# Kernel optimization log

Hardware: AMD Instinct MI355X
Metric: run time of the kernel (lower is better)

The kernel has to match this reference:

```python
import jax, jax.numpy as jnp
import numpy as np

HIDDEN = 512
MEM = 512
COMM = 512
N = 8192


def setup_inputs() -> dict:
    key = jax.random.key(0)
    ks = jax.random.split(key, 8)
    in_dim = HIDDEN + MEM
    s = 1.0 / np.sqrt(in_dim)
    return {
        "u": jax.random.normal(ks[0], (N, HIDDEN), dtype=jnp.float32),
        "z": jax.random.normal(ks[1], (N, MEM), dtype=jnp.float32),
        # torch Linear weights have shape (out, in); biases init to 0 per _init_weights
        "Wk": jax.random.normal(ks[2], (COMM, in_dim), dtype=jnp.float32) * s,
        "bk": jnp.zeros((COMM,), dtype=jnp.float32),
        "Wv": jax.random.normal(ks[3], (COMM, in_dim), dtype=jnp.float32) * s,
        "bv": jnp.zeros((COMM,), dtype=jnp.float32),
        "Wq": jax.random.normal(ks[4], (COMM, in_dim), dtype=jnp.float32) * s,
        "bq": jnp.zeros((COMM,), dtype=jnp.float32),
    }


def reference(u, z, Wk, bk, Wv, bv, Wq, bq):
    n = u.shape[0]
    scale = jnp.sqrt(jnp.asarray(Wk.shape[0], dtype=u.dtype))
    s = jnp.concatenate([u, z], axis=-1)              # (N, in_dim)
    keys = s @ Wk.T + bk                              # (N, C)
    values = s @ Wv.T + bv                            # (N, C)
    queries = s @ Wq.T + bq                           # (N, C)
    scores = (queries @ keys.T) / scale               # (N, N)
    eye = jnp.eye(n, dtype=bool)
    scores = jnp.where(eye, -jnp.inf, scores)         # self-mask
    comm_attn = jax.nn.softmax(scores, axis=-1)
    comm_attn = jnp.nan_to_num(comm_attn, nan=0.0)
    m_bar = comm_attn @ values                        # (N, C)
    return (m_bar, comm_attn)
```

## Files before the change

### kernel.cpp

```cpp
#include <hip/hip_runtime.h>
#include <hip/hip_bf16.h>
#include <stdint.h>

#define N_TOK 8192
#define IN_DIM 1024
#define CDIM 512
#define NW 1536

typedef short bf16x8 __attribute__((ext_vector_type(8)));
typedef float f32x4 __attribute__((ext_vector_type(4)));

__device__ __forceinline__ unsigned short f2bf(float f) {
  union { float f; unsigned int u; } x; x.f = f;
  unsigned int u = x.u;
  u += 0x7fffu + ((u >> 16) & 1u);
  return (unsigned short)(u >> 16);
}

#define GLD16(g, l) __builtin_amdgcn_global_load_lds( \
    (const __attribute__((address_space(1))) void*)(g), \
    (__attribute__((address_space(3))) void*)(l), 16, 0, 0)

__global__ __launch_bounds__(256) void k_convert(
    const float* __restrict__ u, const float* __restrict__ z,
    const float* __restrict__ wk, const float* __restrict__ wv,
    const float* __restrict__ wq,
    ushort* __restrict__ Sb, ushort* __restrict__ Wb) {
  const int S4 = N_TOK * IN_DIM / 4;
  const int W4 = NW * IN_DIM / 4;
  const int total = S4 + W4;
  for (int e = blockIdx.x * blockDim.x + threadIdx.x; e < total;
       e += gridDim.x * blockDim.x) {
    float4 v; ushort* dst;
    if (e < S4) {
      int idx = e << 2; int row = idx >> 10; int col = idx & 1023;
      const float* src = (col < 512) ? (u + row * 512 + col)
                                     : (z + row * 512 + (col - 512));
      v = *(const float4*)src;
      dst = Sb + idx;
    } else {
      int idx = (e - S4) << 2; int row = idx >> 10; int col = idx & 1023;
      const float* base = (row < 512) ? wk : (row < 1024 ? wv : wq);
      v = *(const float4*)(base + (size_t)(row & 511) * 1024 + col);
      dst = Wb + idx;
    }
    ushort4 o;
    o.x = f2bf(v.x); o.y = f2bf(v.y); o.z = f2bf(v.z); o.w = f2bf(v.w);
    *(ushort4*)dst = o;
  }
}

__global__ __launch_bounds__(256) void k_kvq(
    const ushort* __restrict__ Sb, const ushort* __restrict__ Wb,
    const float* __restrict__ bk, const float* __restrict__ bv,
    const float* __restrict__ bq,
    ushort* __restrict__ Kb, ushort* __restrict__ Qb, ushort* __restrict__ VT) {
  __shared__ __align__(16) ushort As[128 * 64];
  __shared__ __align__(16) ushort Bs[128 * 64];
  const int tid = threadIdx.x, lane = tid & 63, w = tid >> 6;
  const int wr = w >> 1, wc = w & 1;
  const int tm = blockIdx.x, tn = blockIdx.y;

  f32x4 acc[4][4];
#pragma unroll
  for (int m = 0; m < 4; m++)
#pragma unroll
    for (int n = 0; n < 4; n++) acc[m][n] = (f32x4){0.f, 0.f, 0.f, 0.f};

  const ushort* ga0 = Sb + (size_t)tm * 128 * IN_DIM;
  const ushort* gb0 = Wb + (size_t)tn * 128 * IN_DIM;

  for (int k0 = 0; k0 < IN_DIM; k0 += 64) {
#pragma unroll
    for (int i = 0; i < 4; i++) {
      int e = i * 256 + tid;
      int row = e >> 3, c8 = (e & 7) << 3;
      GLD16(ga0 + (size_t)row * IN_DIM + k0 + c8, As + e * 8);
      GLD16(gb0 + (size_t)row * IN_DIM + k0 + c8, Bs + e * 8);
    }
    __syncthreads();
#pragma unroll
    for (int kb = 0; kb < 2; kb++) {
      bf16x8 af[4], bfr[4];
#pragma unroll
      for (int m = 0; m < 4; m++)
        af[m] = *(const bf16x8*)(As + (wr * 64 + m * 16 + (lane & 15)) * 64 +
                                 kb * 32 + ((lane >> 4) << 3));
#pragma unroll
      for (int n = 0; n < 4; n++)
        bfr[n] = *(const bf16x8*)(Bs + (wc * 64 + n * 16 + (lane & 15)) * 64 +
                                  kb * 32 + ((lane >> 4) << 3));
#pragma unroll
      for (int m = 0; m < 4; m++)
#pragma unroll
        for (int n = 0; n < 4; n++)
          acc[m][n] = __builtin_amdgcn_mfma_f32_16x16x32_bf16(af[m], bfr[n],
                                                              acc[m][n], 0, 0, 0);
    }
    __syncthreads();
  }

  const int region = tn >> 2;
  const int colr = (tn & 3) * 128 + wc * 64;
  const int rbase = tm * 128 + wr * 64;
  const float* bias = (region == 0) ? bk : (region == 1 ? bv : bq);
  if (region == 1) {
#pragma unroll
    for (int m = 0; m < 4; m++) {
      int r0 = rbase + m * 16 + ((lane >> 4) << 2);
#pragma unroll
      for (int n = 0; n < 4; n++) {
        int c = colr + n * 16 + (lane & 15);
        float b = bias[c];
        ushort4 pk;
        pk.x = f2bf(acc[m][n][0] + b);
        pk.y = f2bf(acc[m][n][1] + b);
        pk.z = f2bf(acc[m][n][2] + b);
        pk.w = f2bf(acc[m][n][3] + b);
        *(ushort4*)(VT + (size_t)c * N_TOK + r0) = pk;
      }
    }
  } else {
    ushort* O = (region == 0) ? Kb : Qb;
#pragma unroll
    for (int m = 0; m < 4; m++) {
      int r0 = rbase + m * 16 + ((lane >> 4) << 2);
#pragma unroll
      for (int n = 0; n < 4; n++) {
        int c = colr + n * 16 + (lane & 15);
        float b = bias[c];
#pragma unroll
        for (int rg = 0; rg < 4; rg++)
          O[(size_t)(r0 + rg) * CDIM + c] = f2bf(acc[m][n][rg] + b);
      }
    }
  }
}

__global__ __launch_bounds__(256) void k_scores(
    const ushort* __restrict__ Qb, const ushort* __restrict__ Kb,
    float* __restrict__ E, float* __restrict__ rowpart) {
  __shared__ __align__(16) ushort As[128 * 64];
  __shared__ __align__(16) ushort Bs[128 * 64];
  __shared__ float sums[256];
  const int tid = threadIdx.x, lane = tid & 63, w = tid >> 6;
  const int wr = w >> 1, wc = w & 1;
  const int tm = blockIdx.x, tn = blockIdx.y;

  f32x4 acc[4][4];
#pragma unroll
  for (int m = 0; m < 4; m++)
#pragma unroll
    for (int n = 0; n < 4; n++) acc[m][n] = (f32x4){0.f, 0.f, 0.f, 0.f};

  const ushort* ga0 = Qb + (size_t)tm * 128 * CDIM;
  const ushort* gb0 = Kb + (size_t)tn * 128 * CDIM;

  for (int k0 = 0; k0 < CDIM; k0 += 64) {
#pragma unroll
    for (int i = 0; i < 4; i++) {
      int e = i * 256 + tid;
      int row = e >> 3, c8 = (e & 7) << 3;
      GLD16(ga0 + (size_t)row * CDIM + k0 + c8, As + e * 8);
      GLD16(gb0 + (size_t)row * CDIM + k0 + c8, Bs + e * 8);
    }
    __syncthreads();
#pragma unroll
    for (int kb = 0; kb < 2; kb++) {
      bf16x8 af[4], bfr[4];
#pragma unroll
      for (int m = 0; m < 4; m++)
        af[m] = *(const bf16x8*)(As + (wr * 64 + m * 16 + (lane & 15)) * 64 +
                                 kb * 32 + ((lane >> 4) << 3));
#pragma unroll
      for (int n = 0; n < 4; n++)
        bfr[n] = *(const bf16x8*)(Bs + (wc * 64 + n * 16 + (lane & 15)) * 64 +
                                  kb * 32 + ((lane >> 4) << 3));
#pragma unroll
      for (int m = 0; m < 4; m++)
#pragma unroll
        for (int n = 0; n < 4; n++)
          acc[m][n] = __builtin_amdgcn_mfma_f32_16x16x32_bf16(af[m], bfr[n],
                                                              acc[m][n], 0, 0, 0);
    }
    __syncthreads();
  }

  const float scale = 0.044194173824159216f;
  float rs[4][4];
#pragma unroll
  for (int m = 0; m < 4; m++)
#pragma unroll
    for (int rg = 0; rg < 4; rg++) rs[m][rg] = 0.f;

#pragma unroll
  for (int m = 0; m < 4; m++) {
    int grow_b = tm * 128 + wr * 64 + m * 16 + ((lane >> 4) << 2);
#pragma unroll
    for (int n = 0; n < 4; n++) {
      int gcol = tn * 128 + wc * 64 + n * 16 + (lane & 15);
#pragma unroll
      for (int rg = 0; rg < 4; rg++) {
        int grow = grow_b + rg;
        float ev = (grow == gcol) ? 0.0f : __expf(acc[m][n][rg] * scale);
        E[(size_t)grow * N_TOK + gcol] = ev;
        rs[m][rg] += ev;
      }
    }
  }
#pragma unroll
  for (int m = 0; m < 4; m++)
#pragma unroll
    for (int rg = 0; rg < 4; rg++) {
      float s = rs[m][rg];
      s += __shfl_xor(s, 1);
      s += __shfl_xor(s, 2);
      s += __shfl_xor(s, 4);
      s += __shfl_xor(s, 8);
      rs[m][rg] = s;
    }
  if ((lane & 15) == 0) {
#pragma unroll
    for (int m = 0; m < 4; m++)
#pragma unroll
      for (int rg = 0; rg < 4; rg++)
        sums[wc * 128 + wr * 64 + m * 16 + ((lane >> 4) << 2) + rg] = rs[m][rg];
  }
  __syncthreads();
  if (tid < 128)
    rowpart[(size_t)(tm * 128 + tid) * 64 + tn] = sums[tid] + sums[128 + tid];
}

__global__ __launch_bounds__(256) void k_rcp(const float* __restrict__ rowpart,
                                             float* __restrict__ rcp_l) {
  int row = blockIdx.x * blockDim.x + threadIdx.x;
  if (row < N_TOK) {
    const float4* p = (const float4*)(rowpart + (size_t)row * 64);
    float s = 0.f;
#pragma unroll
    for (int i = 0; i < 16; i++) {
      float4 v = p[i];
      s += v.x + v.y + v.z + v.w;
    }
    rcp_l[row] = 1.0f / s;
  }
}

__global__ __launch_bounds__(512) void k_attn_pv(
    float* __restrict__ EA,
    const ushort* __restrict__ VT, const float* __restrict__ rcp_l,
    float* __restrict__ part) {
  __shared__ __align__(16) ushort Ps[64 * 64];
  const int tid = threadIdx.x, lane = tid & 63, w = tid >> 6;
  const int rb = blockIdx.x * 64;
  const int jc = blockIdx.y;
  const size_t jbase = (size_t)jc * 4096;

  f32x4 acc[4][4];
#pragma unroll
  for (int m = 0; m < 4; m++)
#pragma unroll
    for (int n = 0; n < 4; n++) acc[m][n] = (f32x4){0.f, 0.f, 0.f, 0.f};

  const int lrow = tid >> 3;
  const int tr = tid & 7;
  const float rl = rcp_l[rb + lrow];
  float* erow = EA + (size_t)(rb + lrow) * N_TOK + jbase + tr * 8;

  float4 e0 = *(const float4*)(erow);
  float4 e1 = *(const float4*)(erow + 4);

  for (int jt = 0; jt < 64; ++jt) {
    float4 p0, p1;
    p0.x = e0.x * rl; p0.y = e0.y * rl; p0.z = e0.z * rl; p0.w = e0.w * rl;
    p1.x = e1.x * rl; p1.y = e1.y * rl; p1.z = e1.z * rl; p1.w = e1.w * rl;
    *(float4*)(erow + jt * 64) = p0;
    *(float4*)(erow + jt * 64 + 4) = p1;
    bf16x8 pb;
    pb[0] = (short)f2bf(p0.x); pb[1] = (short)f2bf(p0.y);
    pb[2] = (short)f2bf(p0.z); pb[3] = (short)f2bf(p0.w);
    pb[4] = (short)f2bf(p1.x); pb[5] = (short)f2bf(p1.y);
    pb[6] = (short)f2bf(p1.z); pb[7] = (short)f2bf(p1.w);

    bf16x8 bfr[2][4];
#pragma unroll
    for (int kb = 0; kb < 2; kb++)
#pragma unroll
      for (int n = 0; n < 4; n++)
        bfr[kb][n] = *(const bf16x8*)(VT +
            (size_t)(w * 64 + n * 16 + (lane & 15)) * N_TOK + jbase +
            jt * 64 + kb * 32 + ((lane >> 4) << 3));

    __syncthreads();
    {
      int chunk = tr ^ (lrow & 7);
      *(bf16x8*)(Ps + lrow * 64 + chunk * 8) = pb;
    }
    __syncthreads();

    if (jt < 63) {
      e0 = *(const float4*)(erow + (jt + 1) * 64);
      e1 = *(const float4*)(erow + (jt + 1) * 64 + 4);
    }

#pragma unroll
    for (int kb = 0; kb < 2; kb++) {
      bf16x8 af[4];
#pragma unroll
      for (int m = 0; m < 4; m++) {
        int r = m * 16 + (lane & 15);
        int chunk = (kb * 4 + (lane >> 4)) ^ (r & 7);
        af[m] = *(const bf16x8*)(Ps + r * 64 + chunk * 8);
      }
#pragma unroll
      for (int m = 0; m < 4; m++)
#pragma unroll
        for (int n = 0; n < 4; n++)
          acc[m][n] = __builtin_amdgcn_mfma_f32_16x16x32_bf16(af[m], bfr[kb][n],
                                                              acc[m][n], 0, 0, 0);
    }
  }

  float* P = part + (size_t)jc * N_TOK * CDIM;
#pragma unroll
  for (int m = 0; m < 4; m++) {
    int r0 = rb + m * 16 + ((lane >> 4) << 2);
#pragma unroll
    for (int n = 0; n < 4; n++) {
      int c = w * 64 + n * 16 + (lane & 15);
#pragma unroll
      for (int rg = 0; rg < 4; rg++)
        P[(size_t)(r0 + rg) * CDIM + c] = acc[m][n][rg];
    }
  }
}

__global__ __launch_bounds__(256) void k_reduce(const float* __restrict__ part,
                                                float* __restrict__ mbar) {
  int idx4 = blockIdx.x * blockDim.x + threadIdx.x;
  const int T4 = N_TOK * CDIM / 4;
  if (idx4 < T4) {
    float4 a = ((const float4*)part)[idx4];
    float4 b = ((const float4*)(part + (size_t)N_TOK * CDIM))[idx4];
    float4 o;
    o.x = a.x + b.x; o.y = a.y + b.y; o.z = a.z + b.z; o.w = a.w + b.w;
    ((float4*)mbar)[idx4] = o;
  }
}

extern "C" void kernel_launch(void* const* d_in, const int* in_sizes, int n_in,
                              void* d_out, int out_size, void* d_ws,
                              size_t ws_size, hipStream_t stream) {
  const float* u  = (const float*)d_in[0];
  const float* z  = (const float*)d_in[1];
  const float* Wk = (const float*)d_in[2];
  const float* bk = (const float*)d_in[3];
  const float* Wv = (const float*)d_in[4];
  const float* bv = (const float*)d_in[5];
  const float* Wq = (const float*)d_in[6];
  const float* bq = (const float*)d_in[7];

  float* mbar = (float*)d_out;
  float* attn = (float*)d_out + (size_t)N_TOK * CDIM;

  char* ws = (char*)d_ws;
  ushort* Sb     = (ushort*)(ws + 0);
  ushort* Wb     = (ushort*)(ws + 16777216);
  ushort* Kb     = (ushort*)(ws + 19922944);
  ushort* Qb     = (ushort*)(ws + 28311552);
  float*  part   = (float*)(ws + 0);
  ushort* VT     = (ushort*)(ws + 36700160);
  float*  rcp_l  = (float*)(ws + 45088768);
  float*  rowpart= (float*)(ws + 45121536);

  k_convert<<<dim3(2048), dim3(256), 0, stream>>>(u, z, Wk, Wv, Wq, Sb, Wb);
  k_kvq<<<dim3(64, 12), dim3(256), 0, stream>>>(Sb, Wb, bk, bv, bq, Kb, Qb, VT);
  k_scores<<<dim3(64, 64), dim3(256), 0, stream>>>(Qb, Kb, attn, rowpart);
  k_rcp<<<dim3(32), dim3(256), 0, stream>>>(rowpart, rcp_l);
  k_attn_pv<<<dim3(128, 2), dim3(512), 0, stream>>>(attn, VT, rcp_l, part);
  k_reduce<<<dim3(4096), dim3(256), 0, stream>>>(part, mbar);
}
```

Baseline: 433.0 us.

## Store unnormalized scores as bf16, GEMM PV directly, normalize attn in separate pass

The scores kernel now writes exp-scores as bf16 into a scratch buffer instead of fp32 into the output, roughly halving that write traffic. PV becomes a plain tiled bf16 GEMM over the full key range with 1/l scaling applied in the epilogue, which removes the split-K partials and the reduce kernel. A separate normalize kernel expands the bf16 scores to fp32 and scales them into the attention output. When the workspace is too small, the bf16 buffer is placed in the upper half of the output and converted in shrinking phases so no row is overwritten before it is read. This costs an extra read of the bf16 scores and adds bf16 rounding of both P and the row sums.

Result: faster. 408.1 us (-5.8%).

```diff
diff --git a/kernel.cpp b/kernel.cpp
--- a/kernel.cpp
+++ b/kernel.cpp
@@ -15,6 +15,10 @@
   unsigned int u = x.u;
   u += 0x7fffu + ((u >> 16) & 1u);
   return (unsigned short)(u >> 16);
+}
+__device__ __forceinline__ float bf2f(unsigned short us) {
+  union { unsigned int u; float f; } x; x.u = ((unsigned int)us) << 16;
+  return x.f;
 }
 
 #define GLD16(g, l) __builtin_amdgcn_global_load_lds( \
@@ -73,10 +77,10 @@
   for (int k0 = 0; k0 < IN_DIM; k0 += 64) {
 #pragma unroll
     for (int i = 0; i < 4; i++) {
-      int e = i * 256 + tid;
-      int row = e >> 3, c8 = (e & 7) << 3;
-      GLD16(ga0 + (size_t)row * IN_DIM + k0 + c8, As + e * 8);
-      GLD16(gb0 + (size_t)row * IN_DIM + k0 + c8, Bs + e * 8);
+      int ce = i * 256 + tid;
+      int row = ce >> 3, c8 = (ce & 7) << 3;
+      GLD16(ga0 + (size_t)row * IN_DIM + k0 + c8, As + ce * 8);
+      GLD16(gb0 + (size_t)row * IN_DIM + k0 + c8, Bs + ce * 8);
     }
     __syncthreads();
 #pragma unroll
@@ -139,7 +143,7 @@
 
 __global__ __launch_bounds__(256) void k_scores(
     const ushort* __restrict__ Qb, const ushort* __restrict__ Kb,
-    float* __restrict__ E, float* __restrict__ rowpart) {
+    ushort* __restrict__ E, float* __restrict__ rowpart) {
   __shared__ __align__(16) ushort As[128 * 64];
   __shared__ __align__(16) ushort Bs[128 * 64];
   __shared__ float sums[256];
@@ -159,10 +163,10 @@
   for (int k0 = 0; k0 < CDIM; k0 += 64) {
 #pragma unroll
     for (int i = 0; i < 4; i++) {
-      int e = i * 256 + tid;
-      int row = e >> 3, c8 = (e & 7) << 3;
-      GLD16(ga0 + (size_t)row * CDIM + k0 + c8, As + e * 8);
-      GLD16(gb0 + (size_t)row * CDIM + k0 + c8, Bs + e * 8);
+      int ce = i * 256 + tid;
+      int row = ce >> 3, c8 = (ce & 7) << 3;
+      GLD16(ga0 + (size_t)row * CDIM + k0 + c8, As + ce * 8);
+      GLD16(gb0 + (size_t)row * CDIM + k0 + c8, Bs + ce * 8);
     }
     __syncthreads();
 #pragma unroll
@@ -203,8 +207,9 @@
       for (int rg = 0; rg < 4; rg++) {
         int grow = grow_b + rg;
         float ev = (grow == gcol) ? 0.0f : __expf(acc[m][n][rg] * scale);
-        E[(size_t)grow * N_TOK + gcol] = ev;
-        rs[m][rg] += ev;
+        unsigned short evb = f2bf(ev);
+        E[(size_t)grow * N_TOK + gcol] = evb;
+        rs[m][rg] += bf2f(evb);
       }
     }
   }
@@ -246,105 +251,121 @@
   }
 }
 
-__global__ __launch_bounds__(512) void k_attn_pv(
-    float* __restrict__ EA,
-    const ushort* __restrict__ VT, const float* __restrict__ rcp_l,
-    float* __restrict__ part) {
-  __shared__ __align__(16) ushort Ps[64 * 64];
+__global__ __launch_bounds__(256) void k_pv(
+    const ushort* __restrict__ E, const ushort* __restrict__ VT,
+    const float* __restrict__ rcp_l, float* __restrict__ mbar) {
+  __shared__ __align__(16) ushort As[128 * 64];
+  __shared__ __align__(16) ushort Bs[64 * 64];
   const int tid = threadIdx.x, lane = tid & 63, w = tid >> 6;
-  const int rb = blockIdx.x * 64;
-  const int jc = blockIdx.y;
-  const size_t jbase = (size_t)jc * 4096;
-
-  f32x4 acc[4][4];
+  const int wr = w >> 1, wc = w & 1;
+  const int tm = blockIdx.x, tn = blockIdx.y;
+
+  f32x4 acc[4][2];
 #pragma unroll
   for (int m = 0; m < 4; m++)
 #pragma unroll
-    for (int n = 0; n < 4; n++) acc[m][n] = (f32x4){0.f, 0.f, 0.f, 0.f};
-
-  const int lrow = tid >> 3;
-  const int tr = tid & 7;
-  const float rl = rcp_l[rb + lrow];
-  float* erow = EA + (size_t)(rb + lrow) * N_TOK + jbase + tr * 8;
-
-  float4 e0 = *(const float4*)(erow);
-  float4 e1 = *(const float4*)(erow + 4);
-
-  for (int jt = 0; jt < 64; ++jt) {
-    float4 p0, p1;
-    p0.x = e0.x * rl; p0.y = e0.y * rl; p0.z = e0.z * rl; p0.w = e0.w * rl;
-    p1.x = e1.x * rl; p1.y = e1.y * rl; p1.z = e1.z * rl; p1.w = e1.w * rl;
-    *(float4*)(erow + jt * 64) = p0;
-    *(float4*)(erow + jt * 64 + 4) = p1;
-    bf16x8 pb;
-    pb[0] = (short)f2bf(p0.x); pb[1] = (short)f2bf(p0.y);
-    pb[2] = (short)f2bf(p0.z); pb[3] = (short)f2bf(p0.w);
-    pb[4] = (short)f2bf(p1.x); pb[5] = (short)f2bf(p1.y);
-    pb[6] = (short)f2bf(p1.z); pb[7] = (short)f2bf(p1.w);
-
-    bf16x8 bfr[2][4];
-#pragma unroll
-    for (int kb = 0; kb < 2; kb++)
-#pragma unroll
-      for (int n = 0; n < 4; n++)
-        bfr[kb][n] = *(const bf16x8*)(VT +
-            (size_t)(w * 64 + n * 16 + (lane & 15)) * N_TOK + jbase +
-            jt * 64 + kb * 32 + ((lane >> 4) << 3));
-
-    __syncthreads();
-    {
-      int chunk = tr ^ (lrow & 7);
-      *(bf16x8*)(Ps + lrow * 64 + chunk * 8) = pb;
-    }
-    __syncthreads();
-
-    if (jt < 63) {
-      e0 = *(const float4*)(erow + (jt + 1) * 64);
-      e1 = *(const float4*)(erow + (jt + 1) * 64 + 4);
-    }
-
+    for (int n = 0; n < 2; n++) acc[m][n] = (f32x4){0.f, 0.f, 0.f, 0.f};
+
+  const ushort* ga0 = E + (size_t)tm * 128 * N_TOK;
+  const ushort* gb0 = VT + (size_t)tn * 64 * N_TOK;
+
+  for (int k0 = 0; k0 < N_TOK; k0 += 64) {
+#pragma unroll
+    for (int i = 0; i < 4; i++) {
+      int ce = i * 256 + tid;
+      int row = ce >> 3, c8 = (ce & 7) << 3;
+      GLD16(ga0 + (size_t)row * N_TOK + k0 + c8, As + ce * 8);
+    }
+#pragma unroll
+    for (int i = 0; i < 2; i++) {
+      int ce = i * 256 + tid;
+      int row = ce >> 3, c8 = (ce & 7) << 3;
+      GLD16(gb0 + (size_t)row * N_TOK + k0 + c8, Bs + ce * 8);
+    }
+    __syncthreads();
 #pragma unroll
     for (int kb = 0; kb < 2; kb++) {
-      bf16x8 af[4];
-#pragma unroll
-      for (int m = 0; m < 4; m++) {
-        int r = m * 16 + (lane & 15);
-        int chunk = (kb * 4 + (lane >> 4)) ^ (r & 7);
-        af[m] = *(const bf16x8*)(Ps + r * 64 + chunk * 8);
-      }
-#pragma unroll
-      for (int m = 0; m < 4; m++)
-#pragma unroll
-        for (int n = 0; n < 4; n++)
-          acc[m][n] = __builtin_amdgcn_mfma_f32_16x16x32_bf16(af[m], bfr[kb][n],
+      bf16x8 af[4], bfr[2];
+#pragma unroll
+      for (int m = 0; m < 4; m++)
+        af[m] = *(const bf16x8*)(As + (wr * 64 + m * 16 + (lane & 15)) * 64 +
+                                 kb * 32 + ((lane >> 4) << 3));
+#pragma unroll
+      for (int n = 0; n < 2; n++)
+        bfr[n] = *(const bf16x8*)(Bs + (wc * 32 + n * 16 + (lane & 15)) * 64 +
+                                  kb * 32 + ((lane >> 4) << 3));
+#pragma unroll
+      for (int m = 0; m < 4; m++)
+#pragma unroll
+        for (int n = 0; n < 2; n++)
+          acc[m][n] = __builtin_amdgcn_mfma_f32_16x16x32_bf16(af[m], bfr[n],
                                                               acc[m][n], 0, 0, 0);
     }
-  }
-
-  float* P = part + (size_t)jc * N_TOK * CDIM;
+    __syncthreads();
+  }
+
 #pragma unroll
   for (int m = 0; m < 4; m++) {
-    int r0 = rb + m * 16 + ((lane >> 4) << 2);
-#pragma unroll
-    for (int n = 0; n < 4; n++) {
-      int c = w * 64 + n * 16 + (lane & 15);
+    int r0 = tm * 128 + wr * 64 + m * 16 + ((lane >> 4) << 2);
+#pragma unroll
+    for (int n = 0; n < 2; n++) {
+      int c = tn * 64 + wc * 32 + n * 16 + (lane & 15);
 #pragma unroll
       for (int rg = 0; rg < 4; rg++)
-        P[(size_t)(r0 + rg) * CDIM + c] = acc[m][n][rg];
-    }
-  }
-}
-
-__global__ __launch_bounds__(256) void k_reduce(const float* __restrict__ part,
-                                                float* __restrict__ mbar) {
-  int idx4 = blockIdx.x * blockDim.x + threadIdx.x;
-  const int T4 = N_TOK * CDIM / 4;
-  if (idx4 < T4) {
-    float4 a = ((const float4*)part)[idx4];
-    float4 b = ((const float4*)(part + (size_t)N_TOK * CDIM))[idx4];
-    float4 o;
-    o.x = a.x + b.x; o.y = a.y + b.y; o.z = a.z + b.z; o.w = a.w + b.w;
-    ((float4*)mbar)[idx4] = o;
+        mbar[(size_t)(r0 + rg) * CDIM + c] = acc[m][n][rg] * rcp_l[r0 + rg];
+    }
+  }
+}
+
+__global__ __launch_bounds__(256) void k_norm(
+    const ushort* __restrict__ E, float* __restrict__ attn,
+    const float* __restrict__ rcp_l, int row0, int nrows) {
+  const int units = nrows << 10;
+  for (int uidx = blockIdx.x * blockDim.x + threadIdx.x; uidx < units;
+       uidx += gridDim.x * blockDim.x) {
+    int row = row0 + (uidx >> 10);
+    int c8 = (uidx & 1023) << 3;
+    const float rl = rcp_l[row];
+    uint4 ev = *(const uint4*)(E + ((size_t)row << 13) + c8);
+    float4 o0, o1;
+    o0.x = bf2f((unsigned short)(ev.x & 0xffffu)) * rl;
+    o0.y = bf2f((unsigned short)(ev.x >> 16)) * rl;
+    o0.z = bf2f((unsigned short)(ev.y & 0xffffu)) * rl;
+    o0.w = bf2f((unsigned short)(ev.y >> 16)) * rl;
+    o1.x = bf2f((unsigned short)(ev.z & 0xffffu)) * rl;
+    o1.y = bf2f((unsigned short)(ev.z >> 16)) * rl;
+    o1.z = bf2f((unsigned short)(ev.w & 0xffffu)) * rl;
+    o1.w = bf2f((unsigned short)(ev.w >> 16)) * rl;
+    float* op = attn + ((size_t)row << 13) + c8;
+    *(float4*)op = o0;
+    *(float4*)(op + 4) = o1;
+  }
+}
+
+__global__ __launch_bounds__(256) void k_lastrow(
+    const ushort* __restrict__ E, float* __restrict__ attn,
+    const float* __restrict__ rcp_l) {
+  const int row = N_TOK - 1;
+  const int t = threadIdx.x;
+  const float rl = rcp_l[row];
+  const uint4* src = (const uint4*)(E + ((size_t)row << 13)) + t * 4;
+  uint4 r0 = src[0], r1 = src[1], r2 = src[2], r3 = src[3];
+  __syncthreads();
+  float* dst = attn + ((size_t)row << 13) + t * 32;
+  uint4 rr[4] = {r0, r1, r2, r3};
+#pragma unroll
+  for (int q = 0; q < 4; q++) {
+    float4 o0, o1;
+    o0.x = bf2f((unsigned short)(rr[q].x & 0xffffu)) * rl;
+    o0.y = bf2f((unsigned short)(rr[q].x >> 16)) * rl;
+    o0.z = bf2f((unsigned short)(rr[q].y & 0xffffu)) * rl;
+    o0.w = bf2f((unsigned short)(rr[q].y >> 16)) * rl;
+    o1.x = bf2f((unsigned short)(rr[q].z & 0xffffu)) * rl;
+    o1.y = bf2f((unsigned short)(rr[q].z >> 16)) * rl;
+    o1.z = bf2f((unsigned short)(rr[q].w & 0xffffu)) * rl;
+    o1.w = bf2f((unsigned short)(rr[q].w >> 16)) * rl;
+    *(float4*)(dst + q * 8) = o0;
+    *(float4*)(dst + q * 8 + 4) = o1;
   }
 }
 
@@ -364,19 +385,37 @@
   float* attn = (float*)d_out + (size_t)N_TOK * CDIM;
 
   char* ws = (char*)d_ws;
-  ushort* Sb     = (ushort*)(ws + 0);
-  ushort* Wb     = (ushort*)(ws + 16777216);
-  ushort* Kb     = (ushort*)(ws + 19922944);
-  ushort* Qb     = (ushort*)(ws + 28311552);
-  float*  part   = (float*)(ws + 0);
-  ushort* VT     = (ushort*)(ws + 36700160);
-  float*  rcp_l  = (float*)(ws + 45088768);
-  float*  rowpart= (float*)(ws + 45121536);
+  ushort* Kb      = (ushort*)(ws + 0);
+  ushort* Qb      = (ushort*)(ws + 8388608);
+  ushort* VT      = (ushort*)(ws + 16777216);
+  float*  rcp_l   = (float*)(ws + 25165824);
+  float*  rowpart = (float*)(ws + 25198592);
+  ushort* Sb      = (ushort*)(ws + 27295744);
+  ushort* Wb      = (ushort*)(ws + 44072960);
+  const size_t E_WS_OFF = 27295744;
+  const size_t REQ = E_WS_OFF + 134217728;
+  const bool ws_mode = (ws_size >= REQ);
+  ushort* E = ws_mode ? (ushort*)(ws + E_WS_OFF)
+                      : (ushort*)((char*)attn + 134217728);
 
   k_convert<<<dim3(2048), dim3(256), 0, stream>>>(u, z, Wk, Wv, Wq, Sb, Wb);
   k_kvq<<<dim3(64, 12), dim3(256), 0, stream>>>(Sb, Wb, bk, bv, bq, Kb, Qb, VT);
-  k_scores<<<dim3(64, 64), dim3(256), 0, stream>>>(Qb, Kb, attn, rowpart);
+  k_scores<<<dim3(64, 64), dim3(256), 0, stream>>>(Qb, Kb, E, rowpart);
   k_rcp<<<dim3(32), dim3(256), 0, stream>>>(rowpart, rcp_l);
-  k_attn_pv<<<dim3(128, 2), dim3(512), 0, stream>>>(attn, VT, rcp_l, part);
-  k_reduce<<<dim3(4096), dim3(256), 0, stream>>>(part, mbar);
-}
+  k_pv<<<dim3(64, 8), dim3(256), 0, stream>>>(E, VT, rcp_l, mbar);
+
+  if (ws_mode) {
+    k_norm<<<dim3(2048), dim3(256), 0, stream>>>(E, attn, rcp_l, 0, N_TOK);
+  } else {
+    static const int ph[] = {0, 4096, 6144, 7168, 7680, 7936, 8064, 8128,
+                             8160, 8176, 8184, 8188, 8190, 8191};
+    for (int p = 0; p + 1 < (int)(sizeof(ph) / sizeof(ph[0])); ++p) {
+      int a = ph[p], b = ph[p + 1];
+      int units = (b - a) << 10;
+      int blocks = (units + 255) / 256;
+      if (blocks > 2048) blocks = 2048;
+      k_norm<<<dim3(blocks), dim3(256), 0, stream>>>(E, attn, rcp_l, a, b - a);
+    }
+    k_lastrow<<<dim3(1), dim3(256), 0, stream>>>(E, attn, rcp_l);
+  }
+}
```
